# Performance work log

Hardware: AMD Instinct MI355X
Metric: run time of the kernel (lower is better)

The kernel has to match this reference:

```python
import jax, jax.numpy as jnp
import numpy as np

B, S, D, NH = 2, 2048, 2048, 16
HD = D // NH  # 128


def setup_inputs() -> dict:
    key = jax.random.key(0)
    ks = jax.random.split(key, 7)
    s = 1.0 / np.sqrt(D)
    return {
        "hidden_states": jax.random.normal(ks[0], (B, S, D), dtype=jnp.float32),
        "Wq": jax.random.normal(ks[1], (D, D), dtype=jnp.float32) * s,
        "Wk": jax.random.normal(ks[2], (D, D), dtype=jnp.float32) * s,
        "Wv": jax.random.normal(ks[3], (D, D), dtype=jnp.float32) * s,
        "Wo": jax.random.normal(ks[4], (D, D), dtype=jnp.float32) * s,
        # phase projections: hidden -> num_heads (zero-init in the module; use small
        # random values so the phase path is numerically exercised)
        "Wpq": jax.random.normal(ks[5], (D, NH), dtype=jnp.float32) * 0.02,
        "Wpk": jax.random.normal(ks[6], (D, NH), dtype=jnp.float32) * 0.02,
    }


def reference(hidden_states, Wq, Wk, Wv, Wo, Wpq, Wpk):
    x = hidden_states  # [B,S,D]
    # ---- base_attn: standard causal multi-head self-attention ----
    q = (x @ Wq).reshape(B, S, NH, HD).transpose(0, 2, 1, 3)  # [B,H,S,hd]
    k = (x @ Wk).reshape(B, S, NH, HD).transpose(0, 2, 1, 3)
    v = (x @ Wv).reshape(B, S, NH, HD).transpose(0, 2, 1, 3)
    scores = jnp.einsum("bhqd,bhkd->bhqk", q, k) / np.sqrt(HD)  # [B,H,S,S]
    causal = jnp.tril(jnp.ones((S, S), dtype=bool))
    scores = jnp.where(causal, scores, jnp.float32(-1e9))
    probs = jax.nn.softmax(scores, axis=-1)
    ctx = jnp.einsum("bhqk,bhkd->bhqd", probs, v)  # [B,H,S,hd]
    attn_output = ctx.transpose(0, 2, 1, 3).reshape(B, S, D) @ Wo  # [B,S,D]
    # ---- phase modulation ----
    # original: cos(pq[b,q,None,h] - pk[b,None,k,h]).mean(dims=(k,h))  -> [B,S]
    # identity: cos(a-b) = cos a * cos b + sin a * sin b lets us avoid the
    # [B,S,S,H] tensor; the math is identical.
    pq = x @ Wpq  # [B,S,H]
    pk = x @ Wpk  # [B,S,H]
    Ck = jnp.cos(pk).sum(axis=1)  # [B,H]
    Sk = jnp.sin(pk).sum(axis=1)  # [B,H]
    phase_mod = (jnp.cos(pq) * Ck[:, None, :] + jnp.sin(pq) * Sk[:, None, :]).sum(-1) / (S * NH)  # [B,S]
    return attn_output * (1.0 + 0.1 * phase_mod[..., None])
```

## Files before the change

### kernel.cpp

```cpp
#include <hip/hip_runtime.h>
#include <hip/hip_bf16.h>

typedef __attribute__((ext_vector_type(8))) short short8;
typedef __attribute__((ext_vector_type(4))) float f32x4;
typedef __attribute__((ext_vector_type(16))) float f32x16;
typedef __attribute__((ext_vector_type(4))) int i32x4;
typedef unsigned short u16;

#define S_LEN 2048
#define D_DIM 2048
#define NHEAD 16
#define HDIM 128
#define M_ROWS 4096

#define MFMA(a,b,c) __builtin_amdgcn_mfma_f32_16x16x32_bf16(a,b,c,0,0,0)
#define MFMA32(a,b,c) __builtin_amdgcn_mfma_f32_32x32x16_bf16(a,b,c,0,0,0)

__device__ __forceinline__ u16 f2bf(float f) {
  union { float f; unsigned u; } v; v.f = f;
  unsigned r = v.u + 0x7fffu + ((v.u >> 16) & 1u);
  return (u16)(r >> 16);
}

__device__ __forceinline__ void async16(void* lds, const void* g) {
  __builtin_amdgcn_global_load_lds(
      (const __attribute__((address_space(1))) unsigned*)g,
      (__attribute__((address_space(3))) unsigned*)lds, 16, 0, 0);
}

__device__ __forceinline__ unsigned cvtpk(float lo, float hi) {
  unsigned r;
  asm("v_cvt_pk_bf16_f32 %0, %1, %2" : "=v"(r) : "v"(lo), "v"(hi));
  return r;
}
__device__ __forceinline__ void plswap(unsigned& x, unsigned& y) {
  asm("v_permlane32_swap_b32 %0, %1" : "+v"(x), "+v"(y));
}

__global__ void k_cvt_x(const float* __restrict__ x, u16* __restrict__ xb) {
  int i = blockIdx.x * 256 + threadIdx.x;
  float4 v = reinterpret_cast<const float4*>(x)[i];
  ushort4 o;
  o.x = f2bf(v.x); o.y = f2bf(v.y); o.z = f2bf(v.z); o.w = f2bf(v.w);
  reinterpret_cast<ushort4*>(xb)[i] = o;
}

__global__ void k_cvt_wt(const float* __restrict__ W, u16* __restrict__ Wt) {
  __shared__ u16 tile[32][33];
  int n0 = blockIdx.x * 32, k0 = blockIdx.y * 32;
  int tx = threadIdx.x & 31, ty = threadIdx.x >> 5;
#pragma unroll
  for (int i = 0; i < 4; i++)
    tile[ty + i * 8][tx] = f2bf(W[(size_t)(k0 + ty + i * 8) * D_DIM + n0 + tx]);
  __syncthreads();
#pragma unroll
  for (int i = 0; i < 4; i++)
    Wt[(size_t)(n0 + ty + i * 8) * D_DIM + k0 + tx] = tile[tx][ty + i * 8];
}

__global__ void k_vtrans(const u16* __restrict__ V, u16* __restrict__ Vt) {
  __shared__ u16 tile[32][33];
  int s0 = blockIdx.x * 32, d0 = blockIdx.y * 32, bh = blockIdx.z;
  const u16* Vp = V + (size_t)bh * S_LEN * HDIM;
  u16* Vtp = Vt + (size_t)bh * HDIM * S_LEN;
  int tx = threadIdx.x & 31, ty = threadIdx.x >> 5;
#pragma unroll
  for (int i = 0; i < 4; i++)
    tile[ty + i * 8][tx] = Vp[(size_t)(s0 + ty + i * 8) * HDIM + d0 + tx];
  __syncthreads();
#pragma unroll
  for (int i = 0; i < 4; i++)
    Vtp[(size_t)(d0 + ty + i * 8) * S_LEN + s0 + tx] = tile[tx][ty + i * 8];
}

template <int NFRAG, int MODE>
__global__ __launch_bounds__(512, 2) void k_gemm2p(const u16* __restrict__ A,
                                                   const u16* __restrict__ Bt,
                                                   void* __restrict__ outp,
                                                   const float* __restrict__ fac) {
  constexpr int BN = NFRAG * 64;
  constexpr int ASUB = 16384;
  constexpr int BSUB = BN * 64;
  constexpr int BBASE = 4 * ASUB;
  constexpr int LPU = 2 + NFRAG / 2;
  __shared__ __align__(16) char lds[4 * ASUB + 4 * BSUB];
  const int m0 = blockIdx.y * 256, n0 = blockIdx.x * BN;
  const int t = threadIdx.x;
  const int w = t >> 6, l = t & 63;
  const int wr = (w >> 2) * 128, wc = (w & 3) * (BN / 4);
  const int lr = l & 15, lq = l >> 4;
  const char* Ab = (const char*)A;
  const char* Bb = (const char*)Bt;

  f32x4 acc[8][NFRAG] = {};

  auto stage_unit = [&](int tt, int s, int buf) {
#pragma unroll
    for (int j = 0; j < 2; j++) {
      const int p = j * 8192 + w * 1024 + l * 16;
      const int row = p >> 6, slot = (p >> 4) & 3;
      async16(lds + buf * 2 * ASUB + s * ASUB + j * 8192 + w * 1024,
              Ab + (size_t)(m0 + row) * 4096 + tt * 128 + s * 64 +
                  ((slot ^ ((row >> 1) & 3)) * 16));
    }
#pragma unroll
    for (int j = 0; j < NFRAG / 2; j++) {
      const int p = j * 8192 + w * 1024 + l * 16;
      const int row = p >> 6, slot = (p >> 4) & 3;
      async16(lds + BBASE + buf * 2 * BSUB + s * BSUB + j * 8192 + w * 1024,
              Bb + (size_t)(n0 + row) * 4096 + tt * 128 + s * 64 +
                  ((slot ^ ((row >> 1) & 3)) * 16));
    }
  };

  auto phase = [&](int buf, int s) {
    const char* Ar = lds + buf * 2 * ASUB + s * ASUB;
    const char* Br = lds + BBASE + buf * 2 * BSUB + s * BSUB;
    short8 af[8], bf[NFRAG];
#pragma unroll
    for (int mi = 0; mi < 8; mi++) {
      const int row = wr + mi * 16 + lr;
      af[mi] = *reinterpret_cast<const short8*>(
          Ar + row * 64 + ((lq ^ ((row >> 1) & 3)) * 16));
    }
#pragma unroll
    for (int ni = 0; ni < NFRAG; ni++) {
      const int row = wc + ni * 16 + lr;
      bf[ni] = *reinterpret_cast<const short8*>(
          Br + row * 64 + ((lq ^ ((row >> 1) & 3)) * 16));
    }
    __builtin_amdgcn_s_setprio(1);
#pragma unroll
    for (int mi = 0; mi < 8; mi++)
#pragma unroll
      for (int ni = 0; ni < NFRAG; ni++)
        acc[mi][ni] = MFMA(af[mi], bf[ni], acc[mi][ni]);
    __builtin_amdgcn_s_setprio(0);
  };

  stage_unit(0, 0, 0);
  stage_unit(0, 1, 0);

  const int NT = D_DIM / 64;
  for (int tt = 0; tt < NT; tt++) {
    const int buf = tt & 1;
    const bool pf = (tt + 1 < NT);
    asm volatile("s_waitcnt vmcnt(%0)" :: "n"(LPU) : "memory");
    __builtin_amdgcn_s_barrier();
    asm volatile("" ::: "memory");
    if (pf) stage_unit(tt + 1, 0, buf ^ 1);
    phase(buf, 0);
    if (pf) asm volatile("s_waitcnt vmcnt(%0)" :: "n"(LPU) : "memory");
    else    asm volatile("s_waitcnt vmcnt(0)" ::: "memory");
    __builtin_amdgcn_s_barrier();
    asm volatile("" ::: "memory");
    if (pf) stage_unit(tt + 1, 1, buf ^ 1);
    phase(buf, 1);
  }

#pragma unroll
  for (int mi = 0; mi < 8; mi++) {
#pragma unroll
    for (int ni = 0; ni < NFRAG; ni++) {
#pragma unroll
      for (int r = 0; r < 4; r++) {
        const int row = m0 + wr + mi * 16 + lq * 4 + r;
        const int col = n0 + wc + ni * 16 + lr;
        const float v = acc[mi][ni][r];
        if (MODE == 0) {
          const int mat = col >> 11;
          const int hh = (col >> 7) & 15;
          ((u16*)outp)[(size_t)mat * 8388608 +
                       (((size_t)((row >> 11) * NHEAD + hh)) * S_LEN + (row & 2047)) * HDIM +
                       (col & 127)] = f2bf(v);
        } else {
          ((float*)outp)[(size_t)row * D_DIM + col] = v * (1.0f + 0.1f * fac[row]);
        }
      }
    }
  }
}

__global__ __launch_bounds__(64) void k_phase_proj(const float* __restrict__ x,
                                                   const float* __restrict__ Wpq,
                                                   const float* __restrict__ Wpk,
                                                   float* __restrict__ pq,
                                                   float* __restrict__ pk) {
  int m = blockIdx.x;
  int l = threadIdx.x;
  int h = l & 15, part = l >> 4;
  const float* xr = x + (size_t)m * D_DIM + part * 512;
  float sq = 0.f, sk = 0.f;
  for (int k = 0; k < 512; k++) {
    float xv = xr[k];
    int kk = part * 512 + k;
    sq += xv * Wpq[(size_t)kk * NHEAD + h];
    sk += xv * Wpk[(size_t)kk * NHEAD + h];
  }
  sq += __shfl_xor(sq, 16); sq += __shfl_xor(sq, 32);
  sk += __shfl_xor(sk, 16); sk += __shfl_xor(sk, 32);
  if (l < 16) {
    pq[(size_t)m * NHEAD + l] = sq;
    pk[(size_t)m * NHEAD + l] = sk;
  }
}

__device__ __forceinline__ float wave_sum(float v) {
  v += __shfl_xor(v, 1);  v += __shfl_xor(v, 2);  v += __shfl_xor(v, 4);
  v += __shfl_xor(v, 8);  v += __shfl_xor(v, 16); v += __shfl_xor(v, 32);
  return v;
}

__global__ void k_phase_ck(const float* __restrict__ pk, float* __restrict__ Ck,
                           float* __restrict__ Sk) {
  int bh = blockIdx.x, b = bh >> 4, h = bh & 15;
  float c = 0.f, s = 0.f;
  for (int ss = threadIdx.x; ss < S_LEN; ss += 256) {
    float v = pk[((size_t)b * S_LEN + ss) * NHEAD + h];
    c += cosf(v); s += sinf(v);
  }
  c = wave_sum(c); s = wave_sum(s);
  __shared__ float rc[4], rs[4];
  int wv = threadIdx.x >> 6;
  if ((threadIdx.x & 63) == 0) { rc[wv] = c; rs[wv] = s; }
  __syncthreads();
  if (threadIdx.x == 0) {
    Ck[bh] = rc[0] + rc[1] + rc[2] + rc[3];
    Sk[bh] = rs[0] + rs[1] + rs[2] + rs[3];
  }
}

__global__ void k_phase_mod(const float* __restrict__ pq, const float* __restrict__ Ck,
                            const float* __restrict__ Sk, float* __restrict__ pm) {
  int m = blockIdx.x * 256 + threadIdx.x;
  int b = m >> 11;
  float a = 0.f;
#pragma unroll
  for (int h = 0; h < NHEAD; h++) {
    float v = pq[(size_t)m * NHEAD + h];
    a += cosf(v) * Ck[b * NHEAD + h] + sinf(v) * Sk[b * NHEAD + h];
  }
  pm[m] = a * (1.0f / (S_LEN * NHEAD));
}

__global__ __launch_bounds__(256, 2) void k_attn(const u16* __restrict__ Q,
                                                 const u16* __restrict__ K,
                                                 const u16* __restrict__ Vt,
                                                 u16* __restrict__ ctx) {
  const int bh = blockIdx.x;
  const int gy = blockIdx.y;
  const int g = (gy < 8) ? (15 - gy) : (gy - 8);
  const int b = bh >> 4, h = bh & 15;
  const int t = threadIdx.x;
  const int w = t >> 6, l = t & 63;
  const int ln = l & 31, hi = l >> 5;
  const int q0w = g * 128 + w * 32;
  const int qq = q0w + ln;
  const float scale = 0.08838834764831845f;

  const u16* Qp = Q + (size_t)bh * S_LEN * HDIM;
  const char* Kg = (const char*)(K + (size_t)bh * S_LEN * HDIM);
  const char* Vg = (const char*)(Vt + (size_t)bh * HDIM * S_LEN);

  __shared__ __align__(16) char Ks[16384];
  __shared__ __align__(16) char Vs[16384];

  short8 qf[8];
#pragma unroll
  for (int c = 0; c < 8; c++)
    qf[c] = *reinterpret_cast<const short8*>(Qp + (size_t)qq * HDIM + c * 16 + hi * 8);

  f32x16 o[4];
#pragma unroll
  for (int ds = 0; ds < 4; ds++)
#pragma unroll
    for (int r = 0; r < 16; r++) o[ds][r] = 0.f;
  float mrun = -1e30f, lsum = 0.f;

  const int kend = (g + 1) * 128;
  for (int k0 = 0; k0 < kend; k0 += 64) {
#pragma unroll
    for (int i = 0; i < 4; i++) {
      const int key = i * 16 + w * 4 + (l >> 4);
      async16(Ks + i * 4096 + w * 1024,
              Kg + (size_t)(k0 + key) * 256 + (((l & 15) * 16) ^ ((key & 15) << 4)));
      const int d = i * 32 + w * 8 + (l >> 3);
      async16(Vs + i * 4096 + w * 1024,
              Vg + (size_t)d * (S_LEN * 2) + k0 * 2 + (((l & 7) * 16) ^ ((d & 7) << 4)));
    }
    __syncthreads();
    if (k0 < q0w + 32) {
      f32x16 s[2];
#pragma unroll
      for (int ks = 0; ks < 2; ks++)
#pragma unroll
        for (int r = 0; r < 16; r++) s[ks][r] = 0.f;
      __builtin_amdgcn_s_setprio(1);
#pragma unroll
      for (int ks = 0; ks < 2; ks++) {
        const int key = ks * 32 + ln;
        const char* kb = Ks + key * 256;
        const unsigned swzk = (unsigned)((key & 15) << 4);
#pragma unroll
        for (int c = 0; c < 8; c++) {
          const short8 kf = *reinterpret_cast<const short8*>(
              kb + (((unsigned)(c * 32 + hi * 16)) ^ swzk));
          s[ks] = MFMA32(kf, qf[c], s[ks]);
        }
      }
      __builtin_amdgcn_s_setprio(0);
      float p[32];
      float mx = -1e30f;
#pragma unroll
      for (int ks = 0; ks < 2; ks++)
#pragma unroll
        for (int r = 0; r < 16; r++) {
          const int key = k0 + ks * 32 + (r & 3) + 8 * (r >> 2) + 4 * hi;
          const float v = (key <= qq) ? s[ks][r] * scale : -1e30f;
          p[ks * 16 + r] = v;
          mx = fmaxf(mx, v);
        }
      mx = fmaxf(mx, __shfl_xor(mx, 32));
      const float nm = fmaxf(mrun, mx);
      const float f = __expf(mrun - nm);
      float rs = 0.f;
#pragma unroll
      for (int i = 0; i < 32; i++) { p[i] = __expf(p[i] - nm); rs += p[i]; }
      rs += __shfl_xor(rs, 32);
      lsum = lsum * f + rs;
      mrun = nm;
#pragma unroll
      for (int ds = 0; ds < 4; ds++)
#pragma unroll
        for (int r = 0; r < 16; r++) o[ds][r] *= f;
      short8 bfr[4];
#pragma unroll
      for (int sub = 0; sub < 2; sub++) {
#pragma unroll
        for (int half = 0; half < 2; half++) {
          const int pb = sub * 16 + half * 8;
          unsigned X1 = cvtpk(p[pb + 0], p[pb + 1]);
          unsigned X2 = cvtpk(p[pb + 2], p[pb + 3]);
          unsigned Y1 = cvtpk(p[pb + 4], p[pb + 5]);
          unsigned Y2 = cvtpk(p[pb + 6], p[pb + 7]);
          plswap(X1, Y1);
          plswap(X2, Y2);
          i32x4 bw;
          bw[0] = (int)X1; bw[1] = (int)X2; bw[2] = (int)Y1; bw[3] = (int)Y2;
          bfr[sub * 2 + half] = __builtin_bit_cast(short8, bw);
        }
      }
      __builtin_amdgcn_s_setprio(1);
#pragma unroll
      for (int ds = 0; ds < 4; ds++) {
        const int d = ds * 32 + ln;
        const char* vb = Vs + d * 128;
        const unsigned swzv = (unsigned)((d & 7) << 4);
#pragma unroll
        for (int slot = 0; slot < 4; slot++) {
          const short8 vf = *reinterpret_cast<const short8*>(
              vb + (((unsigned)(slot * 32 + hi * 16)) ^ swzv));
          o[ds] = MFMA32(vf, bfr[slot], o[ds]);
        }
      }
      __builtin_amdgcn_s_setprio(0);
    }
    __syncthreads();
  }

  const float rl = 1.0f / lsum;
#pragma unroll
  for (int ds = 0; ds < 4; ds++) {
#pragma unroll
    for (int rq = 0; rq < 4; rq++) {
      const int d = ds * 32 + 8 * rq + 4 * hi;
      ushort4 pk4;
      pk4.x = f2bf(o[ds][rq * 4 + 0] * rl);
      pk4.y = f2bf(o[ds][rq * 4 + 1] * rl);
      pk4.z = f2bf(o[ds][rq * 4 + 2] * rl);
      pk4.w = f2bf(o[ds][rq * 4 + 3] * rl);
      *reinterpret_cast<ushort4*>(ctx + ((size_t)(b * S_LEN + qq)) * D_DIM + h * HDIM + d) = pk4;
    }
  }
}

extern "C" void kernel_launch(void* const* d_in, const int* in_sizes, int n_in,
                              void* d_out, int out_size, void* d_ws, size_t ws_size,
                              hipStream_t stream) {
  const float* x   = (const float*)d_in[0];
  const float* Wq  = (const float*)d_in[1];
  const float* Wk  = (const float*)d_in[2];
  const float* Wv  = (const float*)d_in[3];
  const float* Wo  = (const float*)d_in[4];
  const float* Wpq = (const float*)d_in[5];
  const float* Wpk = (const float*)d_in[6];

  char* ws = (char*)d_ws;
  u16* xb   = (u16*)(ws + 0);
  u16* Wqt  = (u16*)(ws + 16777216);
  u16* Wkt  = (u16*)(ws + 25165824);
  u16* Wvt  = (u16*)(ws + 33554432);
  u16* Wot  = (u16*)(ws + 41943040);
  u16* Qb   = (u16*)(ws + 50331648);
  u16* Kb   = (u16*)(ws + 67108864);
  u16* Vb   = (u16*)(ws + 83886080);
  u16* Vt   = (u16*)(ws + 100663296);
  float* pq = (float*)(ws + 117440512);
  float* pk = (float*)(ws + 117702656);
  float* Ck = (float*)(ws + 117964800);
  float* Sk = (float*)(ws + 117964928);
  float* pm = (float*)(ws + 117965056);

  k_cvt_x<<<dim3(M_ROWS * D_DIM / 1024), 256, 0, stream>>>(x, xb);
  k_cvt_wt<<<dim3(64, 64), 256, 0, stream>>>(Wq, Wqt);
  k_cvt_wt<<<dim3(64, 64), 256, 0, stream>>>(Wk, Wkt);
  k_cvt_wt<<<dim3(64, 64), 256, 0, stream>>>(Wv, Wvt);
  k_cvt_wt<<<dim3(64, 64), 256, 0, stream>>>(Wo, Wot);

  k_gemm2p<4, 0><<<dim3(24, 16), 512, 0, stream>>>(xb, Wqt, Qb, nullptr);

  k_vtrans<<<dim3(64, 4, 32), 256, 0, stream>>>(Vb, Vt);

  k_phase_proj<<<dim3(M_ROWS), 64, 0, stream>>>(x, Wpq, Wpk, pq, pk);
  k_phase_ck<<<dim3(32), 256, 0, stream>>>(pk, Ck, Sk);
  k_phase_mod<<<dim3(16), 256, 0, stream>>>(pq, Ck, Sk, pm);

  k_attn<<<dim3(32, 16), 256, 0, stream>>>(Qb, Kb, Vt, Vb );

  k_gemm2p<2, 1><<<dim3(16, 16), 512, 0, stream>>>(Vb , Wot, (void*)d_out, pm);
}
```

Baseline: 327.4 us.

## Deepen GEMM prefetch ring, double-buffer attention K/V, tile phase projection

The GEMM moves from a two-buffer scheme with half-tiles to a four-slot ring of 32-wide K tiles with three tiles in flight, with one barrier per step instead of two. The attention kernel double-buffers its K/V LDS tiles so the next tile's async load overlaps the current compute, and the trailing sync is dropped. The phase projection now reads the bf16 copy of x and stages x rows and the Wpq/Wpk weights through shared memory across 16-row blocks, replacing the per-row scalar loop. Costs are more LDS per block (possibly lower occupancy in attention) and a projection computed from bf16-rounded inputs.

```diff
diff --git a/kernel.cpp b/kernel.cpp
--- a/kernel.cpp
+++ b/kernel.cpp
@@ -74,16 +74,15 @@
 }
 
 template <int NFRAG, int MODE>
-__global__ __launch_bounds__(512, 2) void k_gemm2p(const u16* __restrict__ A,
-                                                   const u16* __restrict__ Bt,
-                                                   void* __restrict__ outp,
-                                                   const float* __restrict__ fac) {
+__global__ __launch_bounds__(512, 2) void k_gemm3(const u16* __restrict__ A,
+                                                  const u16* __restrict__ Bt,
+                                                  void* __restrict__ outp,
+                                                  const float* __restrict__ fac) {
   constexpr int BN = NFRAG * 64;
-  constexpr int ASUB = 16384;
-  constexpr int BSUB = BN * 64;
-  constexpr int BBASE = 4 * ASUB;
+  constexpr int AUNIT = 16384;
+  constexpr int BUNIT = BN * 64;
   constexpr int LPU = 2 + NFRAG / 2;
-  __shared__ __align__(16) char lds[4 * ASUB + 4 * BSUB];
+  __shared__ __align__(16) char lds[4 * (AUNIT + BUNIT)];
   const int m0 = blockIdx.y * 256, n0 = blockIdx.x * BN;
   const int t = threadIdx.x;
   const int w = t >> 6, l = t & 63;
@@ -94,28 +93,28 @@
 
   f32x4 acc[8][NFRAG] = {};
 
-  auto stage_unit = [&](int tt, int s, int buf) {
+  auto stage_unit = [&](int tt) {
+    const int slot = tt & 3;
 #pragma unroll
     for (int j = 0; j < 2; j++) {
       const int p = j * 8192 + w * 1024 + l * 16;
-      const int row = p >> 6, slot = (p >> 4) & 3;
-      async16(lds + buf * 2 * ASUB + s * ASUB + j * 8192 + w * 1024,
-              Ab + (size_t)(m0 + row) * 4096 + tt * 128 + s * 64 +
-                  ((slot ^ ((row >> 1) & 3)) * 16));
+      const int row = p >> 6, sl = (p >> 4) & 3;
+      async16(lds + slot * AUNIT + p,
+              Ab + (size_t)(m0 + row) * 4096 + tt * 64 + ((sl ^ ((row >> 1) & 3)) * 16));
     }
 #pragma unroll
     for (int j = 0; j < NFRAG / 2; j++) {
       const int p = j * 8192 + w * 1024 + l * 16;
-      const int row = p >> 6, slot = (p >> 4) & 3;
-      async16(lds + BBASE + buf * 2 * BSUB + s * BSUB + j * 8192 + w * 1024,
-              Bb + (size_t)(n0 + row) * 4096 + tt * 128 + s * 64 +
-                  ((slot ^ ((row >> 1) & 3)) * 16));
+      const int row = p >> 6, sl = (p >> 4) & 3;
+      async16(lds + 4 * AUNIT + slot * BUNIT + p,
+              Bb + (size_t)(n0 + row) * 4096 + tt * 64 + ((sl ^ ((row >> 1) & 3)) * 16));
     }
   };
 
-  auto phase = [&](int buf, int s) {
-    const char* Ar = lds + buf * 2 * ASUB + s * ASUB;
-    const char* Br = lds + BBASE + buf * 2 * BSUB + s * BSUB;
+  auto compute = [&](int tt) {
+    const int slot = tt & 3;
+    const char* Ar = lds + slot * AUNIT;
+    const char* Br = lds + 4 * AUNIT + slot * BUNIT;
     short8 af[8], bf[NFRAG];
 #pragma unroll
     for (int mi = 0; mi < 8; mi++) {
@@ -138,24 +137,22 @@
     __builtin_amdgcn_s_setprio(0);
   };
 
-  stage_unit(0, 0, 0);
-  stage_unit(0, 1, 0);
-
-  const int NT = D_DIM / 64;
+  stage_unit(0);
+  stage_unit(1);
+  stage_unit(2);
+
+  const int NT = D_DIM / 32;
   for (int tt = 0; tt < NT; tt++) {
-    const int buf = tt & 1;
-    const bool pf = (tt + 1 < NT);
-    asm volatile("s_waitcnt vmcnt(%0)" :: "n"(LPU) : "memory");
+    if (tt < NT - 2)
+      asm volatile("s_waitcnt vmcnt(%0)" :: "n"(2 * LPU) : "memory");
+    else if (tt == NT - 2)
+      asm volatile("s_waitcnt vmcnt(%0)" :: "n"(LPU) : "memory");
+    else
+      asm volatile("s_waitcnt vmcnt(0)" ::: "memory");
     __builtin_amdgcn_s_barrier();
     asm volatile("" ::: "memory");
-    if (pf) stage_unit(tt + 1, 0, buf ^ 1);
-    phase(buf, 0);
-    if (pf) asm volatile("s_waitcnt vmcnt(%0)" :: "n"(LPU) : "memory");
-    else    asm volatile("s_waitcnt vmcnt(0)" ::: "memory");
-    __builtin_amdgcn_s_barrier();
-    asm volatile("" ::: "memory");
-    if (pf) stage_unit(tt + 1, 1, buf ^ 1);
-    phase(buf, 1);
+    if (tt + 3 < NT) stage_unit(tt + 3);
+    compute(tt);
   }
 
 #pragma unroll
@@ -181,28 +178,45 @@
   }
 }
 
-__global__ __launch_bounds__(64) void k_phase_proj(const float* __restrict__ x,
-                                                   const float* __restrict__ Wpq,
-                                                   const float* __restrict__ Wpk,
-                                                   float* __restrict__ pq,
-                                                   float* __restrict__ pk) {
-  int m = blockIdx.x;
-  int l = threadIdx.x;
-  int h = l & 15, part = l >> 4;
-  const float* xr = x + (size_t)m * D_DIM + part * 512;
+__global__ __launch_bounds__(256) void k_phase_proj(const u16* __restrict__ xb,
+                                                    const float* __restrict__ Wpq,
+                                                    const float* __restrict__ Wpk,
+                                                    float* __restrict__ pq,
+                                                    float* __restrict__ pk) {
+  __shared__ u16 xs[16][136];
+  __shared__ float2 ws[128][16];
+  const int t = threadIdx.x;
+  const int m0 = blockIdx.x * 16;
+  const int h = t & 15, r = t >> 4;
   float sq = 0.f, sk = 0.f;
-  for (int k = 0; k < 512; k++) {
-    float xv = xr[k];
-    int kk = part * 512 + k;
-    sq += xv * Wpq[(size_t)kk * NHEAD + h];
-    sk += xv * Wpk[(size_t)kk * NHEAD + h];
-  }
-  sq += __shfl_xor(sq, 16); sq += __shfl_xor(sq, 32);
-  sk += __shfl_xor(sk, 16); sk += __shfl_xor(sk, 32);
-  if (l < 16) {
-    pq[(size_t)m * NHEAD + l] = sq;
-    pk[(size_t)m * NHEAD + l] = sk;
-  }
+  for (int kc = 0; kc < D_DIM; kc += 128) {
+    *reinterpret_cast<short8*>(&xs[t >> 4][(t & 15) * 8]) =
+        *reinterpret_cast<const short8*>(
+            &xb[(size_t)(m0 + (t >> 4)) * D_DIM + kc + (t & 15) * 8]);
+#pragma unroll
+    for (int j = 0; j < 8; j++) {
+      const int idx = j * 256 + t;
+      const int k = idx >> 4, hh = idx & 15;
+      ws[k][hh] = make_float2(Wpq[(size_t)(kc + k) * NHEAD + hh],
+                              Wpk[(size_t)(kc + k) * NHEAD + hh]);
+    }
+    __syncthreads();
+#pragma unroll
+    for (int k8 = 0; k8 < 16; k8++) {
+      const short8 x8 = *reinterpret_cast<const short8*>(&xs[r][k8 * 8]);
+#pragma unroll
+      for (int j = 0; j < 8; j++) {
+        union { float f; unsigned u; } c;
+        c.u = ((unsigned)(u16)x8[j]) << 16;
+        const float2 wv = ws[k8 * 8 + j][h];
+        sq += c.f * wv.x;
+        sk += c.f * wv.y;
+      }
+    }
+    __syncthreads();
+  }
+  pq[(size_t)(m0 + r) * NHEAD + h] = sq;
+  pk[(size_t)(m0 + r) * NHEAD + h] = sk;
 }
 
 __device__ __forceinline__ float wave_sum(float v) {
@@ -262,8 +276,21 @@
   const char* Kg = (const char*)(K + (size_t)bh * S_LEN * HDIM);
   const char* Vg = (const char*)(Vt + (size_t)bh * HDIM * S_LEN);
 
-  __shared__ __align__(16) char Ks[16384];
-  __shared__ __align__(16) char Vs[16384];
+  __shared__ __align__(16) char Ks[2][16384];
+  __shared__ __align__(16) char Vs[2][16384];
+
+  auto stage = [&](int t64, int buf) {
+    const int k0 = t64 * 64;
+#pragma unroll
+    for (int i = 0; i < 4; i++) {
+      const int key = i * 16 + w * 4 + (l >> 4);
+      async16(Ks[buf] + i * 4096 + w * 1024,
+              Kg + (size_t)(k0 + key) * 256 + (((l & 15) * 16) ^ ((key & 15) << 4)));
+      const int d = i * 32 + w * 8 + (l >> 3);
+      async16(Vs[buf] + i * 4096 + w * 1024,
+              Vg + (size_t)d * (S_LEN * 2) + k0 * 2 + (((l & 7) * 16) ^ ((d & 7) << 4)));
+    }
+  };
 
   short8 qf[8];
 #pragma unroll
@@ -277,18 +304,14 @@
     for (int r = 0; r < 16; r++) o[ds][r] = 0.f;
   float mrun = -1e30f, lsum = 0.f;
 
-  const int kend = (g + 1) * 128;
-  for (int k0 = 0; k0 < kend; k0 += 64) {
-#pragma unroll
-    for (int i = 0; i < 4; i++) {
-      const int key = i * 16 + w * 4 + (l >> 4);
-      async16(Ks + i * 4096 + w * 1024,
-              Kg + (size_t)(k0 + key) * 256 + (((l & 15) * 16) ^ ((key & 15) << 4)));
-      const int d = i * 32 + w * 8 + (l >> 3);
-      async16(Vs + i * 4096 + w * 1024,
-              Vg + (size_t)d * (S_LEN * 2) + k0 * 2 + (((l & 7) * 16) ^ ((d & 7) << 4)));
-    }
+  const int nt = (g + 1) * 2;
+  stage(0, 0);
+  for (int t64 = 0; t64 < nt; t64++) {
+    const int buf = t64 & 1;
+    const int k0 = t64 * 64;
+    asm volatile("s_waitcnt vmcnt(0)" ::: "memory");
     __syncthreads();
+    if (t64 + 1 < nt) stage(t64 + 1, buf ^ 1);
     if (k0 < q0w + 32) {
       f32x16 s[2];
 #pragma unroll
@@ -299,7 +322,7 @@
 #pragma unroll
       for (int ks = 0; ks < 2; ks++) {
         const int key = ks * 32 + ln;
-        const char* kb = Ks + key * 256;
+        const char* kb = Ks[buf] + key * 256;
         const unsigned swzk = (unsigned)((key & 15) << 4);
 #pragma unroll
         for (int c = 0; c < 8; c++) {
@@ -354,7 +377,7 @@
 #pragma unroll
       for (int ds = 0; ds < 4; ds++) {
         const int d = ds * 32 + ln;
-        const char* vb = Vs + d * 128;
+        const char* vb = Vs[buf] + d * 128;
         const unsigned swzv = (unsigned)((d & 7) << 4);
 #pragma unroll
         for (int slot = 0; slot < 4; slot++) {
@@ -365,7 +388,6 @@
       }
       __builtin_amdgcn_s_setprio(0);
     }
-    __syncthreads();
   }
 
   const float rl = 1.0f / lsum;
@@ -417,15 +439,15 @@
   k_cvt_wt<<<dim3(64, 64), 256, 0, stream>>>(Wv, Wvt);
   k_cvt_wt<<<dim3(64, 64), 256, 0, stream>>>(Wo, Wot);
 
-  k_gemm2p<4, 0><<<dim3(24, 16), 512, 0, stream>>>(xb, Wqt, Qb, nullptr);
+  k_gemm3<4, 0><<<dim3(24, 16), 512, 0, stream>>>(xb, Wqt, Qb, nullptr);
 
   k_vtrans<<<dim3(64, 4, 32), 256, 0, stream>>>(Vb, Vt);
 
-  k_phase_proj<<<dim3(M_ROWS), 64, 0, stream>>>(x, Wpq, Wpk, pq, pk);
+  k_phase_proj<<<dim3(256), 256, 0, stream>>>(xb, Wpq, Wpk, pq, pk);
   k_phase_ck<<<dim3(32), 256, 0, stream>>>(pk, Ck, Sk);
   k_phase_mod<<<dim3(16), 256, 0, stream>>>(pq, Ck, Sk, pm);
 
   k_attn<<<dim3(32, 16), 256, 0, stream>>>(Qb, Kb, Vt, Vb );
 
-  k_gemm2p<2, 1><<<dim3(16, 16), 512, 0, stream>>>(Vb , Wot, (void*)d_out, pm);
-}
+  k_gemm3<2, 1><<<dim3(16, 16), 512, 0, stream>>>(Vb , Wot, (void*)d_out, pm);
+}
```

Result: slower. 355.3 us (+8.5%).
